# Kernel optimization log

Hardware: AMD Instinct MI355X
Metric: run time of the kernel (lower is better)

The kernel has to match this reference:

```python
import jax, jax.numpy as jnp
import numpy as np

D_MODEL = 1024
NUM_HEADS = 16
HEAD_DIM = D_MODEL // NUM_HEADS
B, S = 4, 2048


def setup_inputs() -> dict:
    key = jax.random.key(0)
    ks = jax.random.split(key, 11)
    s = 1.0 / np.sqrt(D_MODEL)
    return {
        "query": jax.random.normal(ks[0], (B, S, D_MODEL), jnp.float32),
        "key": jax.random.normal(ks[1], (B, S, D_MODEL), jnp.float32),
        "value": jax.random.normal(ks[2], (B, S, D_MODEL), jnp.float32),
        "Wq": jax.random.normal(ks[3], (D_MODEL, D_MODEL), jnp.float32) * s,
        "bq": jnp.zeros((D_MODEL,), jnp.float32),
        "Wk": jax.random.normal(ks[4], (D_MODEL, D_MODEL), jnp.float32) * s,
        "bk": jnp.zeros((D_MODEL,), jnp.float32),
        "Wv": jax.random.normal(ks[5], (D_MODEL, D_MODEL), jnp.float32) * s,
        "bv": jnp.zeros((D_MODEL,), jnp.float32),
        "Wo": jax.random.normal(ks[6], (D_MODEL, D_MODEL), jnp.float32) * s,
        "bo": jnp.zeros((D_MODEL,), jnp.float32),
    }


def _split_heads(x):
    b, s, _ = x.shape
    return x.reshape(b, s, NUM_HEADS, HEAD_DIM).transpose(0, 2, 1, 3)  # [b,h,s,d]


def reference(query, key, value, Wq, bq, Wk, bk, Wv, bv, Wo, bo):
    # torch Linear: y = x @ W.T + b
    q = _split_heads(query @ Wq.T + bq)
    k = _split_heads(key @ Wk.T + bk)
    v = _split_heads(value @ Wv.T + bv)
    scale = 1.0 / jnp.sqrt(jnp.float32(HEAD_DIM))
    scores = jnp.einsum("bhqd,bhkd->bhqk", q, k) * scale
    attn = jax.nn.softmax(scores, axis=-1)
    out = jnp.einsum("bhqk,bhkd->bhqd", attn, v)
    out = out.transpose(0, 2, 1, 3).reshape(query.shape[0], -1, D_MODEL)
    return out @ Wo.T + bo
```

## Files before the change

### kernel.cpp

```cpp
#include <hip/hip_runtime.h>
#include <hip/hip_bf16.h>


typedef __bf16 bf16_t;
typedef __attribute__((ext_vector_type(8))) __bf16 bf16x8;
typedef __attribute__((ext_vector_type(4))) __bf16 bf16x4;
typedef __attribute__((ext_vector_type(4))) float f32x4;

#define MFMA(a, b, c) __builtin_amdgcn_mfma_f32_16x16x32_bf16((a), (b), (c), 0, 0, 0)

__device__ __forceinline__ float fast_exp2(float x) {
#if __has_builtin(__builtin_amdgcn_exp2f)
  return __builtin_amdgcn_exp2f(x);
#else
  return exp2f(x);
#endif
}

__device__ __forceinline__ bf16x8 load8_bf16(const bf16_t* p) {
  return *(const bf16x8*)p;
}
__device__ __forceinline__ bf16x8 load8_bf16(const float* p) {
  f32x4 a = *(const f32x4*)p;
  f32x4 b = *(const f32x4*)(p + 4);
  bf16x8 r;
  for (int i = 0; i < 4; ++i) { r[i] = (bf16_t)a[i]; r[i + 4] = (bf16_t)b[i]; }
  return r;
}

__device__ __forceinline__ void gload_lds16(const bf16_t* g, bf16_t* l) {
  __builtin_amdgcn_global_load_lds(
      (const __attribute__((address_space(1))) void*)g,
      (__attribute__((address_space(3))) void*)l, 16, 0, 0);
}

__global__ __launch_bounds__(256) void convert_bf16(
    const float* __restrict__ xq, const float* __restrict__ xk, const float* __restrict__ xv,
    const float* __restrict__ wq, const float* __restrict__ wk, const float* __restrict__ wv,
    const float* __restrict__ wo,
    bf16_t* __restrict__ xqb, bf16_t* __restrict__ xkb, bf16_t* __restrict__ xvb,
    bf16_t* __restrict__ wqb, bf16_t* __restrict__ wkb, bf16_t* __restrict__ wvb,
    bf16_t* __restrict__ wob) {
  const float* s;
  bf16_t* d;
  size_t n;
  switch (blockIdx.y) {
    case 0: s = xq; d = xqb; n = 8388608; break;
    case 1: s = xk; d = xkb; n = 8388608; break;
    case 2: s = xv; d = xvb; n = 8388608; break;
    case 3: s = wq; d = wqb; n = 1048576; break;
    case 4: s = wk; d = wkb; n = 1048576; break;
    case 5: s = wv; d = wvb; n = 1048576; break;
    default: s = wo; d = wob; n = 1048576; break;
  }
  size_t idx = ((size_t)blockIdx.x * 256 + threadIdx.x) * 8;
  if (idx < n) *(bf16x8*)&d[idx] = load8_bf16(&s[idx]);
}

template <typename TA, typename TW, typename TC, bool VT, bool QS, bool ASYNC>
__device__ __forceinline__ void gemm_body(const TA* __restrict__ A,
                                          const TW* __restrict__ W,
                                          const float* __restrict__ bia,
                                          TC* __restrict__ C) {
  __shared__ __align__(16) bf16_t sA[128 * 32];
  __shared__ __align__(16) bf16_t sW[128 * 32];
  const int tid = threadIdx.x;
  const int lane = tid & 63;
  const int w = tid >> 6;
  const int ln = lane & 15;
  const int q = lane >> 4;
  const int wm = w >> 1, wn = w & 1;
  const size_t m0 = (size_t)blockIdx.x * 128;
  const size_t n0 = (size_t)blockIdx.y * 128;
  const int r0 = tid >> 2;
  const int ko = (tid & 3) * 8;

  f32x4 zero = {0.f, 0.f, 0.f, 0.f};
  f32x4 acc[4][4];
  for (int i = 0; i < 4; ++i)
    for (int j = 0; j < 4; ++j) acc[i][j] = zero;

  for (int k0 = 0; k0 < 1024; k0 += 32) {
    if (ASYNC) {
      __syncthreads();
      for (int i = 0; i < 2; ++i) {
        int c = w * 64 + i * 256 + lane;
        int row = c >> 2;
        int k2 = (c & 3) * 8;
        gload_lds16((const bf16_t*)A + (m0 + row) * 1024 + k0 + k2,
                    &sA[(w * 64 + i * 256) * 8]);
        gload_lds16((const bf16_t*)W + (n0 + row) * 1024 + k0 + k2,
                    &sW[(w * 64 + i * 256) * 8]);
      }
      __syncthreads();
    } else {
      bf16x8 a0 = load8_bf16(&A[(m0 + r0) * 1024 + k0 + ko]);
      bf16x8 a1 = load8_bf16(&A[(m0 + 64 + r0) * 1024 + k0 + ko]);
      bf16x8 w0 = load8_bf16(&W[(n0 + r0) * 1024 + k0 + ko]);
      bf16x8 w1 = load8_bf16(&W[(n0 + 64 + r0) * 1024 + k0 + ko]);
      __syncthreads();
      *(bf16x8*)&sA[tid * 8] = a0;
      *(bf16x8*)&sA[(tid + 256) * 8] = a1;
      *(bf16x8*)&sW[tid * 8] = w0;
      *(bf16x8*)&sW[(tid + 256) * 8] = w1;
      __syncthreads();
    }

    bf16x8 af[4], bfr[4];
    for (int t = 0; t < 4; ++t)
      af[t] = *(const bf16x8*)&sA[(wm * 64 + t * 16 + ln) * 32 + q * 8];
    for (int t = 0; t < 4; ++t)
      bfr[t] = *(const bf16x8*)&sW[(wn * 64 + t * 16 + ln) * 32 + q * 8];
    for (int tm = 0; tm < 4; ++tm)
      for (int tn = 0; tn < 4; ++tn)
        acc[tm][tn] = MFMA(af[tm], bfr[tn], acc[tm][tn]);
  }

  const float sc = QS ? 0.180336880f : 1.0f;
  for (int tn = 0; tn < 4; ++tn) {
    size_t gc = n0 + wn * 64 + tn * 16 + ln;
    float bv = bia[gc];
    for (int tm = 0; tm < 4; ++tm) {
      size_t gr0 = m0 + wm * 64 + tm * 16 + q * 4;
      if (VT) {
        size_t bidx = gr0 >> 11, s0 = gr0 & 2047;
        size_t h = gc >> 6, d = gc & 63;
        bf16x4 pk;
        for (int r = 0; r < 4; ++r) pk[r] = (bf16_t)(acc[tm][tn][r] + bv);
        *(bf16x4*)&((bf16_t*)C)[((bidx * 16 + h) * 64 + d) * 2048 + s0] = pk;
      } else {
        for (int r = 0; r < 4; ++r) {
          float v = (acc[tm][tn][r] + bv) * sc;
          C[(gr0 + r) * 1024 + gc] = (TC)v;
        }
      }
    }
  }
}

__global__ __launch_bounds__(256) void gemm_qkv_b(
    const bf16_t* __restrict__ Xq, const bf16_t* __restrict__ Xk, const bf16_t* __restrict__ Xv,
    const bf16_t* __restrict__ Wq, const bf16_t* __restrict__ Wk, const bf16_t* __restrict__ Wv,
    const float* __restrict__ Bq, const float* __restrict__ Bk, const float* __restrict__ Bv,
    bf16_t* __restrict__ Oq, bf16_t* __restrict__ Ok, bf16_t* __restrict__ Ov) {
  if (blockIdx.z == 0)      gemm_body<bf16_t, bf16_t, bf16_t, false, true , true>(Xq, Wq, Bq, Oq);
  else if (blockIdx.z == 1) gemm_body<bf16_t, bf16_t, bf16_t, false, false, true>(Xk, Wk, Bk, Ok);
  else                      gemm_body<bf16_t, bf16_t, bf16_t, true , false, true>(Xv, Wv, Bv, Ov);
}
__global__ __launch_bounds__(256) void gemm_out_b(
    const bf16_t* __restrict__ A, const bf16_t* __restrict__ W,
    const float* __restrict__ bia, float* __restrict__ C) {
  gemm_body<bf16_t, bf16_t, float, false, false, true>(A, W, bia, C);
}

__global__ __launch_bounds__(256) void gemm_qkv_f(
    const float* __restrict__ Xq, const float* __restrict__ Xk, const float* __restrict__ Xv,
    const float* __restrict__ Wq, const float* __restrict__ Wk, const float* __restrict__ Wv,
    const float* __restrict__ Bq, const float* __restrict__ Bk, const float* __restrict__ Bv,
    bf16_t* __restrict__ Oq, bf16_t* __restrict__ Ok, bf16_t* __restrict__ Ov) {
  if (blockIdx.z == 0)      gemm_body<float, float, bf16_t, false, true , false>(Xq, Wq, Bq, Oq);
  else if (blockIdx.z == 1) gemm_body<float, float, bf16_t, false, false, false>(Xk, Wk, Bk, Ok);
  else                      gemm_body<float, float, bf16_t, true , false, false>(Xv, Wv, Bv, Ov);
}
__global__ __launch_bounds__(256) void gemm_out_f(
    const bf16_t* __restrict__ A, const float* __restrict__ W,
    const float* __restrict__ bia, float* __restrict__ C) {
  gemm_body<bf16_t, float, float, false, false, false>(A, W, bia, C);
}

__global__ __launch_bounds__(512, 4) void flash_attn(const bf16_t* __restrict__ Q,
                                                     const bf16_t* __restrict__ K,
                                                     const bf16_t* __restrict__ Vt,
                                                     bf16_t* __restrict__ O) {
  __shared__ __align__(16) bf16_t sQP[256 * 68];
  __shared__ __align__(16) bf16_t sK[64 * 68];
  __shared__ __align__(16) bf16_t sVt[64 * 68];

  const int tid = threadIdx.x;
  const int lane = tid & 63;
  const int w = tid >> 6;
  const int ln = lane & 15;
  const int q = lane >> 4;
  const int bh = blockIdx.y;
  const int b = bh >> 4;
  const int h = bh & 15;
  const int q0 = blockIdx.x * 256;

  const bf16_t* Qb = Q + ((size_t)b * 2048 + q0) * 1024 + h * 64;
  const bf16_t* Kb = K + ((size_t)b * 2048) * 1024 + h * 64;
  const bf16_t* VtB = Vt + (size_t)bh * 64 * 2048;

  const int krow = tid >> 3;
  const int koff = (tid & 7) * 8;

  bf16x8 kreg = *(const bf16x8*)&Kb[(size_t)krow * 1024 + koff];
  bf16x8 vreg = *(const bf16x8*)&VtB[(size_t)krow * 2048 + koff];

  for (int i = 0; i < 4; ++i) {
    int c = tid + 512 * i;
    int row = c >> 3;
    int off = (c & 7) * 8;
    *(bf16x8*)&sQP[row * 68 + off] = *(const bf16x8*)&Qb[(size_t)row * 1024 + off];
  }
  __syncthreads();
  bf16x8 qf[2][2];
  for (int rc = 0; rc < 2; ++rc)
    for (int kk = 0; kk < 2; ++kk)
      qf[rc][kk] = *(const bf16x8*)&sQP[(w * 32 + rc * 16 + ln) * 68 + kk * 32 + q * 8];
  bf16_t* sP = &sQP[w * 32 * 68];

  f32x4 zero = {0.f, 0.f, 0.f, 0.f};
  f32x4 oacc[2][4];
  for (int rc = 0; rc < 2; ++rc)
    for (int t = 0; t < 4; ++t) oacc[rc][t] = zero;
  float lpart[2][4] = {{0.f, 0.f, 0.f, 0.f}, {0.f, 0.f, 0.f, 0.f}};

  for (int j0 = 0; j0 < 2048; j0 += 64) {
    __syncthreads();
    *(bf16x8*)&sK[krow * 68 + koff] = kreg;
    *(bf16x8*)&sVt[krow * 68 + koff] = vreg;
    __syncthreads();

    if (j0 + 64 < 2048) {
      kreg = *(const bf16x8*)&Kb[(size_t)(j0 + 64 + krow) * 1024 + koff];
      vreg = *(const bf16x8*)&VtB[(size_t)krow * 2048 + (j0 + 64) + koff];
    }

    f32x4 sacc[2][4];
    for (int rc = 0; rc < 2; ++rc)
      for (int tn = 0; tn < 4; ++tn) sacc[rc][tn] = zero;
    for (int kk = 0; kk < 2; ++kk)
      for (int tn = 0; tn < 4; ++tn) {
        bf16x8 kf = *(const bf16x8*)&sK[(tn * 16 + ln) * 68 + kk * 32 + q * 8];
        sacc[0][tn] = MFMA(qf[0][kk], kf, sacc[0][tn]);
        sacc[1][tn] = MFMA(qf[1][kk], kf, sacc[1][tn]);
      }

    for (int rc = 0; rc < 2; ++rc)
      for (int tn = 0; tn < 4; ++tn)
        for (int r = 0; r < 4; ++r) {
          float p = fast_exp2(sacc[rc][tn][r]);
          lpart[rc][r] += p;
          sP[(rc * 16 + q * 4 + r) * 68 + tn * 16 + ln] = (bf16_t)p;
        }

    for (int kk = 0; kk < 2; ++kk) {
      bf16x8 pf0 = *(const bf16x8*)&sP[(size_t)ln * 68 + kk * 32 + q * 8];
      bf16x8 pf1 = *(const bf16x8*)&sP[(size_t)(16 + ln) * 68 + kk * 32 + q * 8];
      for (int tn = 0; tn < 4; ++tn) {
        bf16x8 vf = *(const bf16x8*)&sVt[(tn * 16 + ln) * 68 + kk * 32 + q * 8];
        oacc[0][tn] = MFMA(pf0, vf, oacc[0][tn]);
        oacc[1][tn] = MFMA(pf1, vf, oacc[1][tn]);
      }
    }
  }

  for (int m = 1; m < 16; m <<= 1)
    for (int rc = 0; rc < 2; ++rc)
      for (int r = 0; r < 4; ++r) lpart[rc][r] += __shfl_xor(lpart[rc][r], m);

  bf16_t* Ob = O + ((size_t)b * 2048 + q0 + w * 32) * 1024 + h * 64;
  for (int rc = 0; rc < 2; ++rc)
    for (int r = 0; r < 4; ++r) {
      float inv = 1.f / lpart[rc][r];
      for (int tn = 0; tn < 4; ++tn)
        Ob[(size_t)(rc * 16 + q * 4 + r) * 1024 + tn * 16 + ln] =
            (bf16_t)(oacc[rc][tn][r] * inv);
    }
}

extern "C" void kernel_launch(void* const* d_in, const int* in_sizes, int n_in,
                              void* d_out, int out_size, void* d_ws, size_t ws_size,
                              hipStream_t stream) {
  (void)in_sizes; (void)n_in; (void)out_size;
  const float* query = (const float*)d_in[0];
  const float* key   = (const float*)d_in[1];
  const float* value = (const float*)d_in[2];
  const float* Wq = (const float*)d_in[3];
  const float* bq = (const float*)d_in[4];
  const float* Wk = (const float*)d_in[5];
  const float* bk = (const float*)d_in[6];
  const float* Wv = (const float*)d_in[7];
  const float* bv = (const float*)d_in[8];
  const float* Wo = (const float*)d_in[9];
  const float* bo = (const float*)d_in[10];
  float* out = (float*)d_out;

  const size_t MD = (size_t)8192 * 1024;
  const size_t WD = (size_t)1024 * 1024;
  bf16_t* base = (bf16_t*)d_ws;
  bf16_t* Qw  = base;
  bf16_t* Kw  = Qw + MD;
  bf16_t* Vtw = Kw + MD;

  dim3 b256(256), b512(512);
  if (ws_size >= (6 * MD + 4 * WD) * sizeof(bf16_t)) {
    bf16_t* XqB = Vtw + MD;
    bf16_t* XkB = XqB + MD;
    bf16_t* XvB = XkB + MD;
    bf16_t* WqB = XvB + MD;
    bf16_t* WkB = WqB + WD;
    bf16_t* WvB = WkB + WD;
    bf16_t* WoB = WvB + WD;
    bf16_t* AO  = XqB;

    convert_bf16<<<dim3(4096, 7), b256, 0, stream>>>(
        query, key, value, Wq, Wk, Wv, Wo,
        XqB, XkB, XvB, WqB, WkB, WvB, WoB);
    gemm_qkv_b<<<dim3(64, 8, 3), b256, 0, stream>>>(
        XqB, XkB, XvB, WqB, WkB, WvB, bq, bk, bv, Qw, Kw, Vtw);
    flash_attn<<<dim3(8, 64), b512, 0, stream>>>(Qw, Kw, Vtw, AO);
    gemm_out_b<<<dim3(64, 8), b256, 0, stream>>>(AO, WoB, bo, out);
  } else {
    bf16_t* AO = Vtw + MD;
    gemm_qkv_f<<<dim3(64, 8, 3), b256, 0, stream>>>(
        query, key, value, Wq, Wk, Wv, bq, bk, bv, Qw, Kw, Vtw);
    flash_attn<<<dim3(8, 64), b512, 0, stream>>>(Qw, Kw, Vtw, AO);
    gemm_out_f<<<dim3(64, 8), b256, 0, stream>>>(AO, Wo, bo, out);
  }
}
```

Before: 404.2 us.

## Switch flash attention to 32x32 MFMA with transposed scores kept in registers

Rewrites the attention inner loop to use 32x32x16 bf16 MFMA. Scores are computed as K·Q^T, so each lane's exponentiated probabilities already form the A operand of the P·V MFMA. This removes the LDS round-trip for P and its shared-memory writes and reads, and leaves one row-sum per lane, reduced through a small shared buffer at the end. In exchange it uses larger accumulators (more VGPRs, which could affect occupancy under launch_bounds(512,4)) and splits V fragment loads into two 4-element reads. The softmax still relies on the pre-existing no-max-subtraction exp2 path (scale presumably folded into Q upstream).

```diff
diff --git a/kernel.cpp b/kernel.cpp
--- a/kernel.cpp
+++ b/kernel.cpp
@@ -6,8 +6,10 @@
 typedef __attribute__((ext_vector_type(8))) __bf16 bf16x8;
 typedef __attribute__((ext_vector_type(4))) __bf16 bf16x4;
 typedef __attribute__((ext_vector_type(4))) float f32x4;
+typedef __attribute__((ext_vector_type(16))) float f32x16;
 
 #define MFMA(a, b, c) __builtin_amdgcn_mfma_f32_16x16x32_bf16((a), (b), (c), 0, 0, 0)
+#define MFMA32(a, b, c) __builtin_amdgcn_mfma_f32_32x32x16_bf16((a), (b), (c), 0, 0, 0)
 
 __device__ __forceinline__ float fast_exp2(float x) {
 #if __has_builtin(__builtin_amdgcn_exp2f)
@@ -172,15 +174,16 @@
                                                      const bf16_t* __restrict__ K,
                                                      const bf16_t* __restrict__ Vt,
                                                      bf16_t* __restrict__ O) {
-  __shared__ __align__(16) bf16_t sQP[256 * 68];
+  __shared__ __align__(16) bf16_t sQ[256 * 68];
   __shared__ __align__(16) bf16_t sK[64 * 68];
   __shared__ __align__(16) bf16_t sVt[64 * 68];
+  __shared__ __align__(16) float sL[256];
 
   const int tid = threadIdx.x;
   const int lane = tid & 63;
   const int w = tid >> 6;
-  const int ln = lane & 15;
-  const int q = lane >> 4;
+  const int c = lane & 31;
+  const int hi = lane >> 5;
   const int bh = blockIdx.y;
   const int b = bh >> 4;
   const int h = bh & 15;
@@ -197,23 +200,23 @@
   bf16x8 vreg = *(const bf16x8*)&VtB[(size_t)krow * 2048 + koff];
 
   for (int i = 0; i < 4; ++i) {
-    int c = tid + 512 * i;
-    int row = c >> 3;
-    int off = (c & 7) * 8;
-    *(bf16x8*)&sQP[row * 68 + off] = *(const bf16x8*)&Qb[(size_t)row * 1024 + off];
+    int cc = tid + 512 * i;
+    int row = cc >> 3;
+    int off = (cc & 7) * 8;
+    *(bf16x8*)&sQ[row * 68 + off] = *(const bf16x8*)&Qb[(size_t)row * 1024 + off];
   }
   __syncthreads();
-  bf16x8 qf[2][2];
-  for (int rc = 0; rc < 2; ++rc)
-    for (int kk = 0; kk < 2; ++kk)
-      qf[rc][kk] = *(const bf16x8*)&sQP[(w * 32 + rc * 16 + ln) * 68 + kk * 32 + q * 8];
-  bf16_t* sP = &sQP[w * 32 * 68];
-
-  f32x4 zero = {0.f, 0.f, 0.f, 0.f};
-  f32x4 oacc[2][4];
-  for (int rc = 0; rc < 2; ++rc)
-    for (int t = 0; t < 4; ++t) oacc[rc][t] = zero;
-  float lpart[2][4] = {{0.f, 0.f, 0.f, 0.f}, {0.f, 0.f, 0.f, 0.f}};
+  bf16x8 qf[4];
+#pragma unroll
+  for (int ck = 0; ck < 4; ++ck)
+    qf[ck] = *(const bf16x8*)&sQ[(w * 32 + c) * 68 + ck * 16 + hi * 8];
+
+  f32x16 oacc[2];
+#pragma unroll
+  for (int dt = 0; dt < 2; ++dt)
+#pragma unroll
+    for (int r = 0; r < 16; ++r) oacc[dt][r] = 0.f;
+  float lpart = 0.f;
 
   for (int j0 = 0; j0 < 2048; j0 += 64) {
     __syncthreads();
@@ -226,47 +229,67 @@
       vreg = *(const bf16x8*)&VtB[(size_t)krow * 2048 + (j0 + 64) + koff];
     }
 
-    f32x4 sacc[2][4];
-    for (int rc = 0; rc < 2; ++rc)
-      for (int tn = 0; tn < 4; ++tn) sacc[rc][tn] = zero;
-    for (int kk = 0; kk < 2; ++kk)
-      for (int tn = 0; tn < 4; ++tn) {
-        bf16x8 kf = *(const bf16x8*)&sK[(tn * 16 + ln) * 68 + kk * 32 + q * 8];
-        sacc[0][tn] = MFMA(qf[0][kk], kf, sacc[0][tn]);
-        sacc[1][tn] = MFMA(qf[1][kk], kf, sacc[1][tn]);
-      }
-
-    for (int rc = 0; rc < 2; ++rc)
-      for (int tn = 0; tn < 4; ++tn)
-        for (int r = 0; r < 4; ++r) {
-          float p = fast_exp2(sacc[rc][tn][r]);
-          lpart[rc][r] += p;
-          sP[(rc * 16 + q * 4 + r) * 68 + tn * 16 + ln] = (bf16_t)p;
+    f32x16 sacc[2];
+#pragma unroll
+    for (int kt = 0; kt < 2; ++kt)
+#pragma unroll
+      for (int r = 0; r < 16; ++r) sacc[kt][r] = 0.f;
+#pragma unroll
+    for (int ck = 0; ck < 4; ++ck) {
+#pragma unroll
+      for (int kt = 0; kt < 2; ++kt) {
+        bf16x8 kf = *(const bf16x8*)&sK[(kt * 32 + c) * 68 + ck * 16 + hi * 8];
+        sacc[kt] = MFMA32(kf, qf[ck], sacc[kt]);
+      }
+    }
+
+#pragma unroll
+    for (int kt = 0; kt < 2; ++kt) {
+      float pe[16];
+#pragma unroll
+      for (int r = 0; r < 16; ++r) {
+        pe[r] = fast_exp2(sacc[kt][r]);
+        lpart += pe[r];
+      }
+      bf16x8 pa[2];
+#pragma unroll
+      for (int e = 0; e < 8; ++e) {
+        pa[0][e] = (bf16_t)pe[e];
+        pa[1][e] = (bf16_t)pe[8 + e];
+      }
+#pragma unroll
+      for (int kc = 0; kc < 2; ++kc) {
+#pragma unroll
+        for (int dt = 0; dt < 2; ++dt) {
+          const bf16_t* vb = &sVt[(dt * 32 + c) * 68 + kt * 32 + kc * 16 + 4 * hi];
+          bf16x4 v0 = *(const bf16x4*)vb;
+          bf16x4 v1 = *(const bf16x4*)(vb + 8);
+          bf16x8 vf = {v0[0], v0[1], v0[2], v0[3], v1[0], v1[1], v1[2], v1[3]};
+          oacc[dt] = MFMA32(pa[kc], vf, oacc[dt]);
         }
-
-    for (int kk = 0; kk < 2; ++kk) {
-      bf16x8 pf0 = *(const bf16x8*)&sP[(size_t)ln * 68 + kk * 32 + q * 8];
-      bf16x8 pf1 = *(const bf16x8*)&sP[(size_t)(16 + ln) * 68 + kk * 32 + q * 8];
-      for (int tn = 0; tn < 4; ++tn) {
-        bf16x8 vf = *(const bf16x8*)&sVt[(tn * 16 + ln) * 68 + kk * 32 + q * 8];
-        oacc[0][tn] = MFMA(pf0, vf, oacc[0][tn]);
-        oacc[1][tn] = MFMA(pf1, vf, oacc[1][tn]);
-      }
-    }
-  }
-
-  for (int m = 1; m < 16; m <<= 1)
-    for (int rc = 0; rc < 2; ++rc)
-      for (int r = 0; r < 4; ++r) lpart[rc][r] += __shfl_xor(lpart[rc][r], m);
-
+      }
+    }
+  }
+
+  lpart += __shfl_xor(lpart, 32);
+  if (hi == 0) sL[w * 32 + c] = lpart;
+
+  f32x4 linv[4];
+#pragma unroll
+  for (int bb = 0; bb < 4; ++bb) {
+    f32x4 ls = *(const f32x4*)&sL[w * 32 + 8 * bb + 4 * hi];
+#pragma unroll
+    for (int j = 0; j < 4; ++j) linv[bb][j] = 1.f / ls[j];
+  }
   bf16_t* Ob = O + ((size_t)b * 2048 + q0 + w * 32) * 1024 + h * 64;
-  for (int rc = 0; rc < 2; ++rc)
-    for (int r = 0; r < 4; ++r) {
-      float inv = 1.f / lpart[rc][r];
-      for (int tn = 0; tn < 4; ++tn)
-        Ob[(size_t)(rc * 16 + q * 4 + r) * 1024 + tn * 16 + ln] =
-            (bf16_t)(oacc[rc][tn][r] * inv);
-    }
+#pragma unroll
+  for (int dt = 0; dt < 2; ++dt)
+#pragma unroll
+    for (int bb = 0; bb < 4; ++bb)
+#pragma unroll
+      for (int j = 0; j < 4; ++j)
+        Ob[(size_t)(8 * bb + 4 * hi + j) * 1024 + dt * 32 + c] =
+            (bf16_t)(oacc[dt][4 * bb + j] * linv[bb][j]);
 }
 
 extern "C" void kernel_launch(void* const* d_in, const int* in_sizes, int n_in,
```

Measured after the change: 350.5 us. 13.3% less time.
